# Kernel optimization log

Measured on AMD Instinct MI355X. Metric: run time of the kernel, lower is better.

Reference implementation:

```python
import jax, jax.numpy as jnp
import numpy as np

EMBED_DIM = 2048
NUM_HEADS = 16
HEAD_DIM = EMBED_DIM // NUM_HEADS  # 128
EPS = 1e-12  # F.normalize default eps


def setup_inputs() -> dict:
    key = jax.random.key(0)
    k1, k2, k3 = jax.random.split(key, 3)
    x = jax.random.normal(k1, (4, 2048, EMBED_DIM), dtype=jnp.float32)
    # nn.Linear(embed_dim, 3*embed_dim): weight [3E, E], bias [3E]
    W = jax.random.normal(k2, (3 * EMBED_DIM, EMBED_DIM), dtype=jnp.float32) * (EMBED_DIM ** -0.5)
    b = jax.random.normal(k3, (3 * EMBED_DIM,), dtype=jnp.float32) * 0.02
    return {"x": x, "W": W, "b": b}


def _l2_normalize(t):
    # matches F.normalize(p=2, dim=-1): t / max(||t||, eps)
    n = jnp.sqrt(jnp.sum(t * t, axis=-1, keepdims=True))
    return t / jnp.maximum(n, EPS)


def reference(x, W, b):
    B, L, E = x.shape
    H, HD = NUM_HEADS, HEAD_DIM
    y = x @ W.T + b  # [B, L, 3E]
    # rearrange '... l (h c) -> ... h l c' with c = 3*HD, then chunk into q,k,v
    y = y.reshape(B, L, H, 3, HD)
    q = jnp.transpose(y[..., 0, :], (0, 2, 1, 3))  # [B, H, L, HD]
    k = jnp.transpose(y[..., 1, :], (0, 2, 1, 3))
    v = jnp.transpose(y[..., 2, :], (0, 2, 1, 3))
    q = _l2_normalize(q)
    k = _l2_normalize(k)
    # cosine attention, scale=1, non-causal, no mask
    scores = jnp.einsum('bhld,bhmd->bhlm', q, k)
    attn = jax.nn.softmax(scores, axis=-1)
    out = jnp.einsum('bhlm,bhmd->bhld', attn, v)  # [B, H, L, HD]
    return jnp.transpose(out, (0, 2, 1, 3)).reshape(B, L, E)
```

## Files before the change

kernel.cpp:

```cpp
#include <hip/hip_runtime.h>
#include <hip/hip_bf16.h>

typedef __bf16 bf16_t;
typedef __bf16 bf16x8 __attribute__((ext_vector_type(8)));
typedef __bf16 bf16x4 __attribute__((ext_vector_type(4)));
typedef __bf16 bf16x2 __attribute__((ext_vector_type(2)));
typedef float f32x4 __attribute__((ext_vector_type(4)));

#define MFMA16(a,b,c) __builtin_amdgcn_mfma_f32_16x16x32_bf16((a),(b),(c),0,0,0)
#define AS3(p) ((__attribute__((address_space(3))) void*)(p))
#define AS1(p) ((const __attribute__((address_space(1))) void*)(p))

constexpr int B_ = 4, L_ = 2048, E_ = 2048, H_ = 16, HD_ = 128;
constexpr size_t QK_ELEMS = (size_t)B_ * H_ * L_ * HD_;
constexpr size_t NX = (size_t)B_ * L_ * E_;
constexpr size_t NW = (size_t)3 * E_ * E_;

__global__ __launch_bounds__(256) void cvt(
    const float* __restrict__ X, const float* __restrict__ W, bf16_t* __restrict__ dst)
{
  size_t e = ((size_t)blockIdx.x * 256 + threadIdx.x) * 4;
  f32x4 v = (e < NX) ? *(const f32x4*)&X[e] : *(const f32x4*)&W[e - NX];
  bf16x4 o;
  for (int u = 0; u < 4; ++u) o[u] = (__bf16)v[u];
  *(bf16x4*)&dst[e] = o;
}

__global__ __launch_bounds__(256) void gemm_qkv(
    const bf16_t* __restrict__ Xb, const bf16_t* __restrict__ Wb, const float* __restrict__ bias,
    bf16_t* __restrict__ q, bf16_t* __restrict__ k, bf16_t* __restrict__ vT)
{
  __shared__ alignas(16) bf16_t As[128 * 32];
  __shared__ alignas(16) bf16_t Bs[128 * 32];
  const int tid = threadIdx.x;
  const int wave = tid >> 6, lane = tid & 63;
  const int wm = wave >> 1, wn = wave & 1;
  const int m0 = blockIdx.y * 128, n0 = blockIdx.x * 128;
  const int rowf = lane & 15, kq8 = (lane >> 4) * 8;

  const int srow = wave * 32 + (lane >> 2);
  const int scol = (lane & 3) * 8;
  const bf16_t* gA0 = &Xb[(size_t)(m0 + srow) * E_ + scol];
  const bf16_t* gB0 = &Wb[(size_t)(n0 + srow) * E_ + scol];
  bf16_t* lA0 = &As[(wave * 32) * 32];
  bf16_t* lA1 = &As[(wave * 32 + 16) * 32];
  bf16_t* lB0 = &Bs[(wave * 32) * 32];
  bf16_t* lB1 = &Bs[(wave * 32 + 16) * 32];

  const f32x4 fzero = {0.f, 0.f, 0.f, 0.f};
  f32x4 acc[4][4];
  for (int i = 0; i < 4; ++i)
    for (int j = 0; j < 4; ++j) acc[i][j] = fzero;

  for (int k0 = 0; k0 < E_; k0 += 32) {
    __syncthreads();
    __builtin_amdgcn_global_load_lds(AS1(gA0 + k0),            AS3(lA0), 16, 0, 0);
    __builtin_amdgcn_global_load_lds(AS1(gA0 + 16 * E_ + k0),  AS3(lA1), 16, 0, 0);
    __builtin_amdgcn_global_load_lds(AS1(gB0 + k0),            AS3(lB0), 16, 0, 0);
    __builtin_amdgcn_global_load_lds(AS1(gB0 + 16 * E_ + k0),  AS3(lB1), 16, 0, 0);
    __syncthreads();
    bf16x8 af[4], bfr[4];
    for (int mt = 0; mt < 4; ++mt) af[mt]  = *(const bf16x8*)&As[(wm * 64 + mt * 16 + rowf) * 32 + kq8];
    for (int nt = 0; nt < 4; ++nt) bfr[nt] = *(const bf16x8*)&Bs[(wn * 64 + nt * 16 + rowf) * 32 + kq8];
    for (int mt = 0; mt < 4; ++mt)
      for (int nt = 0; nt < 4; ++nt)
        acc[mt][nt] = MFMA16(af[mt], bfr[nt], acc[mt][nt]);
  }

  const int b  = m0 >> 11;
  const int l0 = m0 & (L_ - 1);
  const int h  = n0 / 384;
  const int which = (n0 % 384) >> 7;

  float bcol[4];
  for (int nt = 0; nt < 4; ++nt)
    bcol[nt] = bias[n0 + wn * 64 + nt * 16 + (lane & 15)];

  if (which < 2) {
    bf16_t* base = ((which == 0) ? q : k) + ((size_t)(b * H_ + h) * L_) * HD_;
    for (int mt = 0; mt < 4; ++mt)
      for (int r = 0; r < 4; ++r) {
        int l = l0 + wm * 64 + mt * 16 + ((lane >> 4) << 2) + r;
        bf16_t* rowp = base + (size_t)l * HD_;
        for (int nt = 0; nt < 4; ++nt) {
          int hd = wn * 64 + nt * 16 + (lane & 15);
          rowp[hd] = (__bf16)(acc[mt][nt][r] + bcol[nt]);
        }
      }
  } else {
    bf16_t* base = vT + ((size_t)(b * H_ + h) * HD_) * L_;
    for (int mt = 0; mt < 4; ++mt)
      for (int r = 0; r < 4; ++r) {
        int l = l0 + wm * 64 + mt * 16 + ((lane >> 4) << 2) + r;
        for (int nt = 0; nt < 4; ++nt) {
          int hd = wn * 64 + nt * 16 + (lane & 15);
          base[(size_t)hd * L_ + l] = (__bf16)(acc[mt][nt][r] + bcol[nt]);
        }
      }
  }
}

__global__ __launch_bounds__(256) void norm_qk(bf16_t* __restrict__ q, bf16_t* __restrict__ kk)
{
  const int gw = blockIdx.x * 4 + (threadIdx.x >> 6);
  const int lane = threadIdx.x & 63;
  const int rows_per = B_ * H_ * L_;
  bf16_t* base = (gw < rows_per) ? q : kk;
  int row = (gw < rows_per) ? gw : gw - rows_per;
  bf16_t* p = base + (size_t)row * HD_ + lane * 2;
  bf16x2 v2 = *(const bf16x2*)p;
  float a = (float)v2.x, bb = (float)v2.y;
  float ss = a * a + bb * bb;
  for (int off = 32; off; off >>= 1) ss += __shfl_xor(ss, off);
  float sc = 1.0f / fmaxf(sqrtf(ss), 1e-12f);
  v2.x = (__bf16)(a * sc);
  v2.y = (__bf16)(bb * sc);
  *(bf16x2*)p = v2;
}

__device__ __forceinline__ int swz128(int r, int c) {
  return r * 128 + ((((c >> 3) ^ (r & 15)) & 15) << 3) + (c & 7);
}
__device__ __forceinline__ int swz64(int r, int c) {
  return r * 64 + ((((c >> 3) ^ (r & 7)) & 7) << 3) + (c & 7);
}

__global__ __launch_bounds__(256) void attn(
    const bf16_t* __restrict__ q, const bf16_t* __restrict__ k,
    const bf16_t* __restrict__ vT, float* __restrict__ out)
{
  __shared__ alignas(16) bf16_t Ks[64 * 128];
  __shared__ alignas(16) bf16_t Vts[128 * 64];
  __shared__ alignas(16) bf16_t Ps[128 * 64];

  const int tid = threadIdx.x, wave = tid >> 6, lane = tid & 63;
  const int bh = blockIdx.y;
  const int q0 = blockIdx.x * 128;
  const int rowf = lane & 15, kq8 = (lane >> 4) * 8;

  const bf16_t* qbase = q + ((size_t)bh * L_ + q0) * HD_;
  const bf16_t* kbh = k + (size_t)bh * L_ * HD_;
  const bf16_t* vbh = vT + (size_t)bh * HD_ * L_;

  bf16x8 qf[4][2];
  for (int kk4 = 0; kk4 < 4; ++kk4)
    for (int mt = 0; mt < 2; ++mt)
      qf[kk4][mt] = *(const bf16x8*)&qbase[(size_t)(wave * 32 + mt * 16 + rowf) * HD_ + kk4 * 32 + kq8];

  const f32x4 fzero = {0.f, 0.f, 0.f, 0.f};
  f32x4 o[2][8];
  for (int mt = 0; mt < 2; ++mt)
    for (int nt = 0; nt < 8; ++nt) o[mt][nt] = fzero;
  float lrow[2][4];
  for (int mt = 0; mt < 2; ++mt)
    for (int r = 0; r < 4; ++r) lrow[mt][r] = 0.f;

  bf16x8 kreg[4], vreg[4];

  for (int i = 0; i < 4; ++i) {
    int e = (i * 256 + tid) * 8;
    kreg[i] = *(const bf16x8*)&kbh[e];
  }
  for (int i = 0; i < 4; ++i) {
    int e = (i * 256 + tid) * 8;
    int d = e >> 6, c = e & 63;
    vreg[i] = *(const bf16x8*)&vbh[(size_t)d * L_ + c];
  }
  for (int i = 0; i < 4; ++i) {
    int e = (i * 256 + tid) * 8;
    *(bf16x8*)&Ks[swz128(e >> 7, e & 127)] = kreg[i];
  }
  for (int i = 0; i < 4; ++i) {
    int e = (i * 256 + tid) * 8;
    int d = e >> 6, c = e & 63;
    *(bf16x8*)&Vts[swz64(d, c)] = vreg[i];
  }
  __syncthreads();

  for (int j0 = 0; j0 < L_; j0 += 64) {
    const bool more = (j0 + 64 < L_);
    if (more) {
      const int jn = j0 + 64;
      for (int i = 0; i < 4; ++i) {
        int e = (i * 256 + tid) * 8;
        kreg[i] = *(const bf16x8*)&kbh[(size_t)jn * HD_ + e];
      }
      for (int i = 0; i < 4; ++i) {
        int e = (i * 256 + tid) * 8;
        int d = e >> 6, c = e & 63;
        vreg[i] = *(const bf16x8*)&vbh[(size_t)d * L_ + jn + c];
      }
    }

    f32x4 s[2][4];
    for (int mt = 0; mt < 2; ++mt)
      for (int nt = 0; nt < 4; ++nt) s[mt][nt] = fzero;
    __builtin_amdgcn_s_setprio(1);
    for (int kk = 0; kk < 128; kk += 32) {
      bf16x8 bk4[4];
      for (int nt = 0; nt < 4; ++nt) bk4[nt] = *(const bf16x8*)&Ks[swz128(nt * 16 + rowf, kk + kq8)];
      for (int mt = 0; mt < 2; ++mt)
        for (int nt = 0; nt < 4; ++nt)
          s[mt][nt] = MFMA16(qf[kk >> 5][mt], bk4[nt], s[mt][nt]);
    }
    __builtin_amdgcn_s_setprio(0);

    for (int mt = 0; mt < 2; ++mt)
      for (int nt = 0; nt < 4; ++nt)
        for (int r = 0; r < 4; ++r) {
          float p = __expf(s[mt][nt][r]);
          lrow[mt][r] += p;
          int rr = wave * 32 + mt * 16 + ((lane >> 4) << 2) + r;
          int cc = nt * 16 + (lane & 15);
          Ps[swz64(rr, cc)] = (__bf16)p;
        }

    __builtin_amdgcn_s_setprio(1);
    for (int kk = 0; kk < 64; kk += 32) {
      bf16x8 ap[2];
      for (int mt = 0; mt < 2; ++mt)
        ap[mt] = *(const bf16x8*)&Ps[swz64(wave * 32 + mt * 16 + rowf, kk + kq8)];
      for (int nt = 0; nt < 8; ++nt) {
        bf16x8 bvv = *(const bf16x8*)&Vts[swz64(nt * 16 + rowf, kk + kq8)];
        for (int mt = 0; mt < 2; ++mt)
          o[mt][nt] = MFMA16(ap[mt], bvv, o[mt][nt]);
      }
    }
    __builtin_amdgcn_s_setprio(0);

    __syncthreads();
    if (more) {
      for (int i = 0; i < 4; ++i) {
        int e = (i * 256 + tid) * 8;
        *(bf16x8*)&Ks[swz128(e >> 7, e & 127)] = kreg[i];
      }
      for (int i = 0; i < 4; ++i) {
        int e = (i * 256 + tid) * 8;
        int d = e >> 6, c = e & 63;
        *(bf16x8*)&Vts[swz64(d, c)] = vreg[i];
      }
      __syncthreads();
    }
  }

  const int b = bh >> 4, h = bh & 15;
  for (int mt = 0; mt < 2; ++mt) {
    for (int r = 0; r < 4; ++r) {
      float lsum = lrow[mt][r];
      for (int off = 8; off; off >>= 1) lsum += __shfl_xor(lsum, off);
      float inv = 1.0f / lsum;
      int l = q0 + wave * 32 + mt * 16 + ((lane >> 4) << 2) + r;
      float* op = out + (((size_t)b * L_ + l) * H_ + h) * HD_;
      for (int nt = 0; nt < 8; ++nt) {
        int d = nt * 16 + (lane & 15);
        op[d] = o[mt][nt][r] * inv;
      }
    }
  }
}

extern "C" void kernel_launch(void* const* d_in, const int* in_sizes, int n_in,
                              void* d_out, int out_size, void* d_ws, size_t ws_size,
                              hipStream_t stream)
{
  const float* X    = (const float*)d_in[0];
  const float* W    = (const float*)d_in[1];
  const float* bias = (const float*)d_in[2];
  float* out = (float*)d_out;

  bf16_t* Xb = (bf16_t*)d_out;
  bf16_t* Wb = Xb + NX;

  bf16_t* q  = (bf16_t*)d_ws;
  bf16_t* k  = q + QK_ELEMS;
  bf16_t* vT = k + QK_ELEMS;

  cvt<<<dim3((NX + NW) / (256 * 4)), 256, 0, stream>>>(X, W, Xb);
  gemm_qkv<<<dim3(48, 64), 256, 0, stream>>>(Xb, Wb, bias, q, k, vT);
  norm_qk<<<dim3(65536), 256, 0, stream>>>(q, k);
  attn<<<dim3(16, 64), 256, 0, stream>>>(q, k, vT, out);
}
```

Measured before the change: 683.8 us.

## Double-buffer QKV GEMM loads, fragment-ordered LDS layout, fuse L2 norm into epilogue

Result: slower. 780.3 us (+14.1%).

```diff
diff --git a/kernel.cpp b/kernel.cpp
--- a/kernel.cpp
+++ b/kernel.cpp
@@ -30,92 +30,102 @@
     const bf16_t* __restrict__ Xb, const bf16_t* __restrict__ Wb, const float* __restrict__ bias,
     bf16_t* __restrict__ q, bf16_t* __restrict__ k, bf16_t* __restrict__ vT)
 {
-  __shared__ alignas(16) bf16_t As[128 * 32];
-  __shared__ alignas(16) bf16_t Bs[128 * 32];
+  __shared__ alignas(16) bf16_t As[2][128 * 32];
+  __shared__ alignas(16) bf16_t Bs[2][128 * 32];
   const int tid = threadIdx.x;
   const int wave = tid >> 6, lane = tid & 63;
   const int wm = wave >> 1, wn = wave & 1;
   const int m0 = blockIdx.y * 128, n0 = blockIdx.x * 128;
-  const int rowf = lane & 15, kq8 = (lane >> 4) * 8;
-
-  const int srow = wave * 32 + (lane >> 2);
-  const int scol = (lane & 3) * 8;
-  const bf16_t* gA0 = &Xb[(size_t)(m0 + srow) * E_ + scol];
-  const bf16_t* gB0 = &Wb[(size_t)(n0 + srow) * E_ + scol];
-  bf16_t* lA0 = &As[(wave * 32) * 32];
-  bf16_t* lA1 = &As[(wave * 32 + 16) * 32];
-  bf16_t* lB0 = &Bs[(wave * 32) * 32];
-  bf16_t* lB1 = &Bs[(wave * 32 + 16) * 32];
+
+  const int sr = lane & 15, sq8 = (lane >> 4) * 8;
+  const bf16_t* gA = &Xb[(size_t)(m0 + wave * 32 + sr) * E_ + sq8];
+  const bf16_t* gB = &Wb[(size_t)(n0 + wave * 32 + sr) * E_ + sq8];
+  bf16_t* lA = &As[0][wave * 1024];
+  bf16_t* lB = &Bs[0][wave * 1024];
+
+#define STAGE(c, k0) do { \
+    __builtin_amdgcn_global_load_lds(AS1(gA + (k0)),           AS3(lA + (c) * 4096),       16, 0, 0); \
+    __builtin_amdgcn_global_load_lds(AS1(gA + 16 * E_ + (k0)), AS3(lA + (c) * 4096 + 512), 16, 0, 0); \
+    __builtin_amdgcn_global_load_lds(AS1(gB + (k0)),           AS3(lB + (c) * 4096),       16, 0, 0); \
+    __builtin_amdgcn_global_load_lds(AS1(gB + 16 * E_ + (k0)), AS3(lB + (c) * 4096 + 512), 16, 0, 0); \
+  } while (0)
 
   const f32x4 fzero = {0.f, 0.f, 0.f, 0.f};
   f32x4 acc[4][4];
   for (int i = 0; i < 4; ++i)
     for (int j = 0; j < 4; ++j) acc[i][j] = fzero;
 
-  for (int k0 = 0; k0 < E_; k0 += 32) {
-    __syncthreads();
-    __builtin_amdgcn_global_load_lds(AS1(gA0 + k0),            AS3(lA0), 16, 0, 0);
-    __builtin_amdgcn_global_load_lds(AS1(gA0 + 16 * E_ + k0),  AS3(lA1), 16, 0, 0);
-    __builtin_amdgcn_global_load_lds(AS1(gB0 + k0),            AS3(lB0), 16, 0, 0);
-    __builtin_amdgcn_global_load_lds(AS1(gB0 + 16 * E_ + k0),  AS3(lB1), 16, 0, 0);
-    __syncthreads();
+  STAGE(0, 0);
+  __syncthreads();
+  int cur = 0;
+  for (int t = 0; t < 64; ++t) {
+    if (t < 63) STAGE(cur ^ 1, (t + 1) * 32);
     bf16x8 af[4], bfr[4];
-    for (int mt = 0; mt < 4; ++mt) af[mt]  = *(const bf16x8*)&As[(wm * 64 + mt * 16 + rowf) * 32 + kq8];
-    for (int nt = 0; nt < 4; ++nt) bfr[nt] = *(const bf16x8*)&Bs[(wn * 64 + nt * 16 + rowf) * 32 + kq8];
+    for (int mt = 0; mt < 4; ++mt) af[mt]  = *(const bf16x8*)&As[cur][(wm * 4 + mt) * 512 + lane * 8];
+    for (int nt = 0; nt < 4; ++nt) bfr[nt] = *(const bf16x8*)&Bs[cur][(wn * 4 + nt) * 512 + lane * 8];
+    __builtin_amdgcn_s_setprio(1);
     for (int mt = 0; mt < 4; ++mt)
       for (int nt = 0; nt < 4; ++nt)
         acc[mt][nt] = MFMA16(af[mt], bfr[nt], acc[mt][nt]);
-  }
+    __builtin_amdgcn_s_setprio(0);
+    __syncthreads();
+    cur ^= 1;
+  }
+#undef STAGE
 
   const int b  = m0 >> 11;
   const int l0 = m0 & (L_ - 1);
   const int h  = n0 / 384;
   const int which = (n0 % 384) >> 7;
+  const int rlane = (lane >> 4) << 2;
+  const int clane = lane & 15;
 
   float bcol[4];
   for (int nt = 0; nt < 4; ++nt)
-    bcol[nt] = bias[n0 + wn * 64 + nt * 16 + (lane & 15)];
+    bcol[nt] = bias[n0 + wn * 64 + nt * 16 + clane];
 
   if (which < 2) {
+    float* NormS = (float*)&As[0][0];
+    for (int mt = 0; mt < 4; ++mt)
+      for (int r = 0; r < 4; ++r) {
+        float sq = 0.f;
+        for (int nt = 0; nt < 4; ++nt) {
+          float v = acc[mt][nt][r] + bcol[nt];
+          acc[mt][nt][r] = v;
+          sq += v * v;
+        }
+        for (int off = 8; off; off >>= 1) sq += __shfl_xor(sq, off);
+        if (clane == 0) NormS[(wm * 64 + mt * 16 + rlane + r) * 2 + wn] = sq;
+      }
+    __syncthreads();
+    float invn[4][4];
+    for (int mt = 0; mt < 4; ++mt)
+      for (int r = 0; r < 4; ++r) {
+        int ll = wm * 64 + mt * 16 + rlane + r;
+        float tot = NormS[ll * 2] + NormS[ll * 2 + 1];
+        invn[mt][r] = 1.0f / fmaxf(sqrtf(tot), 1e-12f);
+      }
     bf16_t* base = ((which == 0) ? q : k) + ((size_t)(b * H_ + h) * L_) * HD_;
     for (int mt = 0; mt < 4; ++mt)
       for (int r = 0; r < 4; ++r) {
-        int l = l0 + wm * 64 + mt * 16 + ((lane >> 4) << 2) + r;
+        int l = l0 + wm * 64 + mt * 16 + rlane + r;
         bf16_t* rowp = base + (size_t)l * HD_;
         for (int nt = 0; nt < 4; ++nt) {
-          int hd = wn * 64 + nt * 16 + (lane & 15);
-          rowp[hd] = (__bf16)(acc[mt][nt][r] + bcol[nt]);
+          int hd = wn * 64 + nt * 16 + clane;
+          rowp[hd] = (__bf16)(acc[mt][nt][r] * invn[mt][r]);
         }
       }
   } else {
     bf16_t* base = vT + ((size_t)(b * H_ + h) * HD_) * L_;
     for (int mt = 0; mt < 4; ++mt)
       for (int r = 0; r < 4; ++r) {
-        int l = l0 + wm * 64 + mt * 16 + ((lane >> 4) << 2) + r;
+        int l = l0 + wm * 64 + mt * 16 + rlane + r;
         for (int nt = 0; nt < 4; ++nt) {
-          int hd = wn * 64 + nt * 16 + (lane & 15);
+          int hd = wn * 64 + nt * 16 + clane;
           base[(size_t)hd * L_ + l] = (__bf16)(acc[mt][nt][r] + bcol[nt]);
         }
       }
   }
-}
-
-__global__ __launch_bounds__(256) void norm_qk(bf16_t* __restrict__ q, bf16_t* __restrict__ kk)
-{
-  const int gw = blockIdx.x * 4 + (threadIdx.x >> 6);
-  const int lane = threadIdx.x & 63;
-  const int rows_per = B_ * H_ * L_;
-  bf16_t* base = (gw < rows_per) ? q : kk;
-  int row = (gw < rows_per) ? gw : gw - rows_per;
-  bf16_t* p = base + (size_t)row * HD_ + lane * 2;
-  bf16x2 v2 = *(const bf16x2*)p;
-  float a = (float)v2.x, bb = (float)v2.y;
-  float ss = a * a + bb * bb;
-  for (int off = 32; off; off >>= 1) ss += __shfl_xor(ss, off);
-  float sc = 1.0f / fmaxf(sqrtf(ss), 1e-12f);
-  v2.x = (__bf16)(a * sc);
-  v2.y = (__bf16)(bb * sc);
-  *(bf16x2*)p = v2;
 }
 
 __device__ __forceinline__ int swz128(int r, int c) {
@@ -277,6 +287,5 @@
 
   cvt<<<dim3((NX + NW) / (256 * 4)), 256, 0, stream>>>(X, W, Xb);
   gemm_qkv<<<dim3(48, 64), 256, 0, stream>>>(Xb, Wb, bias, q, k, vT);
-  norm_qk<<<dim3(65536), 256, 0, stream>>>(q, k);
   attn<<<dim3(16, 64), 256, 0, stream>>>(q, k, vT, out);
 }
```
